# Performance work log

Hardware: AMD Instinct MI355X
Metric: run time of the kernel (lower is better)

## Reference

```python
import jax, jax.numpy as jnp
import numpy as np

D_MODEL = 1024
NUM_HEAD = 16
D_K = D_MODEL // NUM_HEAD
FFN_D = 4096
EPS = 1e-5


def _layernorm(x, gamma, beta):
    mu = jnp.mean(x, axis=-1, keepdims=True)
    var = jnp.mean(jnp.square(x - mu), axis=-1, keepdims=True)
    return (x - mu) * jax.lax.rsqrt(var + EPS) * gamma + beta


def setup_inputs() -> dict:
    key = jax.random.key(0)
    ks = jax.random.split(key, 16)
    s = 1.0 / np.sqrt(D_MODEL)
    sf = 1.0 / np.sqrt(FFN_D)
    # weights stored as [in, out] (transpose of torch nn.Linear.weight)
    return {
        "x": jax.random.normal(ks[0], (4, 2048, D_MODEL), dtype=jnp.float32),
        "wq": jax.random.uniform(ks[1], (D_MODEL, D_MODEL), jnp.float32, -s, s),
        "bq": jax.random.uniform(ks[2], (D_MODEL,), jnp.float32, -s, s),
        "wk": jax.random.uniform(ks[3], (D_MODEL, D_MODEL), jnp.float32, -s, s),
        "bk": jax.random.uniform(ks[4], (D_MODEL,), jnp.float32, -s, s),
        "wv": jax.random.uniform(ks[5], (D_MODEL, D_MODEL), jnp.float32, -s, s),
        "bv": jax.random.uniform(ks[6], (D_MODEL,), jnp.float32, -s, s),
        "wo": jax.random.uniform(ks[7], (D_MODEL, D_MODEL), jnp.float32, -s, s),
        "bo": jax.random.uniform(ks[8], (D_MODEL,), jnp.float32, -s, s),
        "w1": jax.random.uniform(ks[9], (D_MODEL, FFN_D), jnp.float32, -s, s),
        "b1": jax.random.uniform(ks[10], (FFN_D,), jnp.float32, -s, s),
        "w2": jax.random.uniform(ks[11], (FFN_D, D_MODEL), jnp.float32, -sf, sf),
        "b2": jax.random.uniform(ks[12], (D_MODEL,), jnp.float32, -sf, sf),
        "g1": jnp.ones((D_MODEL,), jnp.float32),
        "be1": jnp.zeros((D_MODEL,), jnp.float32),
        "g2": jnp.ones((D_MODEL,), jnp.float32),
        "be2": jnp.zeros((D_MODEL,), jnp.float32),
    }


def reference(x, wq, bq, wk, bk, wv, bv, wo, bo, w1, b1, w2, b2, g1, be1, g2, be2):
    B, S, _ = x.shape
    resid1 = x
    # project and split heads: [B, H, S, d_k]
    def heads(w, b):
        return (x @ w + b).reshape(B, S, NUM_HEAD, D_K).transpose(0, 2, 1, 3)
    q = heads(wq, bq)
    k = heads(wk, bk)
    v = heads(wv, bv)
    scores = jnp.einsum("bhsd,bhtd->bhst", q, k) / jnp.sqrt(jnp.float32(D_K))
    attn = jax.nn.softmax(scores, axis=-1)
    ctx = jnp.einsum("bhst,bhtd->bhsd", attn, v)
    ctx = ctx.transpose(0, 2, 1, 3).reshape(B, S, D_MODEL)
    attn_out = ctx @ wo + bo
    x1 = _layernorm(resid1 + attn_out, g1, be1)
    ffn = jax.nn.relu(x1 @ w1 + b1) @ w2 + b2
    return _layernorm(x1 + ffn, g2, be2)
```

## Files before the change

kernel.cpp:

```cpp
#include <hip/hip_runtime.h>

typedef unsigned short u16;
typedef __attribute__((ext_vector_type(8))) u16 u16x8;
typedef __attribute__((ext_vector_type(8))) __bf16 bf16x8;
typedef __attribute__((ext_vector_type(4))) float floatx4;

#define MFMA16(a, b, c) __builtin_amdgcn_mfma_f32_16x16x32_bf16( \
    __builtin_bit_cast(bf16x8, a), __builtin_bit_cast(bf16x8, b), c, 0, 0, 0)

__device__ __forceinline__ float bf2f(u16 h) {
  unsigned u = ((unsigned)h) << 16;
  float f;
  __builtin_memcpy(&f, &u, 4);
  return f;
}
__device__ __forceinline__ u16 f2bf(float f) {
  unsigned u;
  __builtin_memcpy(&u, &f, 4);
  u += 0x7fff + ((u >> 16) & 1);
  return (u16)(u >> 16);
}
__device__ __forceinline__ u16 f2bf_rtz(float f) {
  unsigned u;
  __builtin_memcpy(&u, &f, 4);
  return (u16)(u >> 16);
}

typedef __attribute__((address_space(1))) const unsigned int gas_u32;
typedef __attribute__((address_space(3))) unsigned int las_u32;

__device__ __forceinline__ void gld_lds16(const u16* g, u16* l) {
  __builtin_amdgcn_global_load_lds((gas_u32*)g, (las_u32*)l, 16, 0, 0);
}

__global__ __launch_bounds__(256) void transpose_k(const float* __restrict__ in,
                                                   u16* __restrict__ out, int R, int C) {
  __shared__ u16 tile[64][65];
  int c0 = blockIdx.x * 64, r0 = blockIdx.y * 64;
  int tc = threadIdx.x & 63, tr = threadIdx.x >> 6;
#pragma unroll
  for (int i = 0; i < 16; ++i)
    tile[tr + i * 4][tc] = f2bf(in[(size_t)(r0 + tr + i * 4) * C + c0 + tc]);
  __syncthreads();
#pragma unroll
  for (int i = 0; i < 16; ++i)
    out[(size_t)(c0 + tr + i * 4) * R + r0 + tc] = tile[tc][tr + i * 4];
}

__global__ __launch_bounds__(256) void vtrans_k(const u16* __restrict__ V,
                                                u16* __restrict__ VtG) {
  __shared__ u16 tile[64][65];
  int t0 = blockIdx.x * 64;
  int bh = blockIdx.y, b = bh >> 4, h = bh & 15;
  int tc = threadIdx.x & 63, tr = threadIdx.x >> 6;
#pragma unroll
  for (int i = 0; i < 16; ++i)
    tile[tr + i * 4][tc] = V[((size_t)(b * 2048 + t0 + tr + i * 4)) * 1024 + h * 64 + tc];
  __syncthreads();
#pragma unroll
  for (int i = 0; i < 16; ++i)
    VtG[((size_t)(bh * 64 + tr + i * 4)) * 2048 + t0 + tc] = tile[tc][tr + i * 4];
}

__global__ __launch_bounds__(256) void convert_k(const float* __restrict__ in,
                                                 u16* __restrict__ out) {
  size_t idx = ((size_t)blockIdx.x * 256 + threadIdx.x) * 8;
  floatx4 f0 = *(const floatx4*)(in + idx);
  floatx4 f1 = *(const floatx4*)(in + idx + 4);
  u16x8 o;
#pragma unroll
  for (int e = 0; e < 4; ++e) o[e] = f2bf(f0[e]);
#pragma unroll
  for (int e = 0; e < 4; ++e) o[4 + e] = f2bf(f1[e]);
  *(u16x8*)(out + idx) = o;
}

template <bool C_F32>
__global__ __launch_bounds__(256, 2) void gemm_bt(const u16* __restrict__ A,
                                                  const u16* __restrict__ BT,
                                                  const float* __restrict__ bias,
                                                  void* __restrict__ Cv, int M, int N, int K,
                                                  int relu) {
  __shared__ __align__(16) u16 As[128 * 32];
  __shared__ __align__(16) u16 Bs[128 * 32];
  const int tid = threadIdx.x, lane = tid & 63, wave = tid >> 6;
  const int quad = lane >> 4, l15 = lane & 15;
  const int wr = wave >> 1, wc = wave & 1;
  const int m0 = blockIdx.x * 128, n0 = blockIdx.y * 128;

  floatx4 acc[4][4] = {};

  for (int k0 = 0; k0 < K; k0 += 32) {
#pragma unroll
    for (int p = 0; p < 2; ++p) {
      int chunk = p * 256 + tid;
      int row = chunk >> 2, cc = chunk & 3;
      int ldsbase = (p * 256 + wave * 64) * 8;
      gld_lds16(A + (size_t)(m0 + row) * K + k0 + cc * 8, As + ldsbase);
      gld_lds16(BT + (size_t)(n0 + row) * K + k0 + cc * 8, Bs + ldsbase);
    }
    __syncthreads();
    u16x8 af[4], bfr[4];
#pragma unroll
    for (int i = 0; i < 4; ++i)
      af[i] = *(const u16x8*)(As + (wr * 64 + i * 16 + l15) * 32 + quad * 8);
#pragma unroll
    for (int j = 0; j < 4; ++j)
      bfr[j] = *(const u16x8*)(Bs + (wc * 64 + j * 16 + l15) * 32 + quad * 8);
#pragma unroll
    for (int i = 0; i < 4; ++i)
#pragma unroll
      for (int j = 0; j < 4; ++j) acc[i][j] = MFMA16(af[i], bfr[j], acc[i][j]);
    __syncthreads();
  }

#pragma unroll
  for (int j = 0; j < 4; ++j) {
    int col = n0 + wc * 64 + j * 16 + l15;
    float bv = bias[col];
#pragma unroll
    for (int i = 0; i < 4; ++i) {
      int row = m0 + wr * 64 + i * 16 + quad * 4;
#pragma unroll
      for (int r = 0; r < 4; ++r) {
        float v = acc[i][j][r] + bv;
        if (relu) v = fmaxf(v, 0.f);
        if (C_F32)
          ((float*)Cv)[(size_t)(row + r) * N + col] = v;
        else
          ((u16*)Cv)[(size_t)(row + r) * N + col] = f2bf(v);
      }
    }
  }
}

__global__ __launch_bounds__(256, 2) void attn_k(const u16* __restrict__ Q,
                                                 const u16* __restrict__ Km,
                                                 const u16* __restrict__ VtG,
                                                 u16* __restrict__ O) {
  __shared__ __align__(16) u16 Qs[128 * 72];
  __shared__ __align__(16) u16 Ks[2][64 * 64];
  __shared__ __align__(16) u16 Vs[2][64 * 64];
  const int tid = threadIdx.x, lane = tid & 63, wave = tid >> 6;
  const int quad = lane >> 4, l15 = lane & 15;
  const int b = blockIdx.z, h = blockIdx.y, q0 = blockIdx.x * 128;
  const int bh = b * 16 + h;
  const size_t tokbase = (size_t)b * 2048;

#pragma unroll
  for (int p = 0; p < 4; ++p) {
    int chunk = p * 256 + tid, row = chunk >> 3, cc = chunk & 7;
    u16x8 qv = *(const u16x8*)(Q + (tokbase + q0 + row) * 1024 + h * 64 + cc * 8);
#pragma unroll
    for (int e = 0; e < 8; ++e) qv[e] = f2bf(bf2f(qv[e]) * 0.125f);
    *(u16x8*)(Qs + row * 72 + cc * 8) = qv;
  }
  __syncthreads();
  u16x8 qa[2][2];
#pragma unroll
  for (int i = 0; i < 2; ++i)
#pragma unroll
    for (int ks = 0; ks < 2; ++ks)
      qa[i][ks] = *(const u16x8*)(Qs + (wave * 32 + i * 16 + l15) * 72 + ks * 32 + quad * 8);
  __syncthreads();
  u16* Ps = Qs;

  floatx4 o[2][4] = {};
  float lsum[2][4] = {};

  auto stage = [&](int it2, int buf) {
    int t0 = it2 * 64;
#pragma unroll
    for (int p = 0; p < 2; ++p) {
      int chunk = p * 256 + tid;
      int row = chunk >> 3, cc = chunk & 7;
      int gc = cc ^ (row & 7);
      int ldsoff = (p * 256 + wave * 64) * 8;
      gld_lds16(Km + (tokbase + t0 + row) * 1024 + h * 64 + gc * 8, &Ks[buf][ldsoff]);
      gld_lds16(VtG + ((size_t)(bh * 64 + row)) * 2048 + t0 + gc * 8, &Vs[buf][ldsoff]);
    }
  };

  stage(0, 0);

  for (int it = 0; it < 32; ++it) {
    const int cur = it & 1;
    __syncthreads();
    if (it + 1 < 32) stage(it + 1, cur ^ 1);

    floatx4 s[2][4] = {};
#pragma unroll
    for (int ks = 0; ks < 2; ++ks) {
      u16x8 kb[4];
#pragma unroll
      for (int j = 0; j < 4; ++j)
        kb[j] = *(const u16x8*)(&Ks[cur][(j * 16 + l15) * 64 + (((ks * 4 + quad) ^ (l15 & 7)) * 8)]);
#pragma unroll
      for (int i = 0; i < 2; ++i)
#pragma unroll
        for (int j = 0; j < 4; ++j) s[i][j] = MFMA16(qa[i][ks], kb[j], s[i][j]);
    }

#pragma unroll
    for (int i = 0; i < 2; ++i)
#pragma unroll
      for (int r = 0; r < 4; ++r) {
        int prow = wave * 32 + i * 16 + quad * 4 + r;
        float ls = 0.f;
#pragma unroll
        for (int j = 0; j < 4; ++j) {
          float p = __expf(s[i][j][r]);
          ls += p;
          Ps[prow * 72 + j * 16 + l15] = f2bf_rtz(p);
        }
        lsum[i][r] += ls;
      }
    asm volatile("s_waitcnt lgkmcnt(0)\n\ts_barrier" ::: "memory");

#pragma unroll
    for (int ks = 0; ks < 2; ++ks) {
      u16x8 pa[2], vbf[4];
#pragma unroll
      for (int i = 0; i < 2; ++i)
        pa[i] = *(const u16x8*)(Ps + (wave * 32 + i * 16 + l15) * 72 + ks * 32 + quad * 8);
#pragma unroll
      for (int jd = 0; jd < 4; ++jd)
        vbf[jd] = *(const u16x8*)(&Vs[cur][(jd * 16 + l15) * 64 + (((ks * 4 + quad) ^ (l15 & 7)) * 8)]);
#pragma unroll
      for (int i = 0; i < 2; ++i)
#pragma unroll
        for (int jd = 0; jd < 4; ++jd) o[i][jd] = MFMA16(pa[i], vbf[jd], o[i][jd]);
    }
  }

#pragma unroll
  for (int i = 0; i < 2; ++i) {
    float inv[4];
#pragma unroll
    for (int r = 0; r < 4; ++r) {
      float v = lsum[i][r];
#pragma unroll
      for (int mk = 1; mk < 16; mk <<= 1) v += __shfl_xor(v, mk);
      inv[r] = 1.0f / fmaxf(v, 1e-30f);
    }
#pragma unroll
    for (int jd = 0; jd < 4; ++jd)
#pragma unroll
      for (int r = 0; r < 4; ++r) {
        float val = o[i][jd][r] * inv[r];
        size_t tok = tokbase + q0 + wave * 32 + i * 16 + quad * 4 + r;
        O[tok * 1024 + h * 64 + jd * 16 + l15] = f2bf(val);
      }
  }
}

template <bool A_F32, bool B_F32, bool OUT_F32>
__global__ __launch_bounds__(256) void ln_k(const void* __restrict__ Av,
                                            const void* __restrict__ Bv,
                                            const float* __restrict__ g,
                                            const float* __restrict__ be,
                                            void* __restrict__ outv) {
  const int lane = threadIdx.x & 63, wave = threadIdx.x >> 6;
  const size_t row = (size_t)blockIdx.x * 4 + wave;
  const size_t base = row * 1024 + lane * 16;
  float v[16];
  if (A_F32) {
    const float* a = (const float*)Av + base;
#pragma unroll
    for (int q = 0; q < 4; ++q) {
      floatx4 t = *(const floatx4*)(a + q * 4);
#pragma unroll
      for (int e = 0; e < 4; ++e) v[q * 4 + e] = t[e];
    }
  } else {
    const u16* a = (const u16*)Av + base;
    u16x8 a0 = *(const u16x8*)a, a1 = *(const u16x8*)(a + 8);
#pragma unroll
    for (int e = 0; e < 8; ++e) {
      v[e] = bf2f(a0[e]);
      v[e + 8] = bf2f(a1[e]);
    }
  }
  if (B_F32) {
    const float* bb = (const float*)Bv + base;
#pragma unroll
    for (int q = 0; q < 4; ++q) {
      floatx4 t = *(const floatx4*)(bb + q * 4);
#pragma unroll
      for (int e = 0; e < 4; ++e) v[q * 4 + e] += t[e];
    }
  } else {
    const u16* bb = (const u16*)Bv + base;
    u16x8 b0 = *(const u16x8*)bb, b1 = *(const u16x8*)(bb + 8);
#pragma unroll
    for (int e = 0; e < 8; ++e) {
      v[e] += bf2f(b0[e]);
      v[e + 8] += bf2f(b1[e]);
    }
  }
  float sum = 0.f, sq = 0.f;
#pragma unroll
  for (int e = 0; e < 16; ++e) {
    sum += v[e];
    sq += v[e] * v[e];
  }
#pragma unroll
  for (int mk = 1; mk < 64; mk <<= 1) {
    sum += __shfl_xor(sum, mk);
    sq += __shfl_xor(sq, mk);
  }
  float mu = sum * (1.f / 1024.f);
  float var = fmaxf(sq * (1.f / 1024.f) - mu * mu, 0.f);
  float rstd = rsqrtf(var + 1e-5f);
  if (OUT_F32) {
    float* o = (float*)outv + base;
#pragma unroll
    for (int q = 0; q < 4; ++q) {
      floatx4 t;
#pragma unroll
      for (int e = 0; e < 4; ++e) {
        int c = lane * 16 + q * 4 + e;
        t[e] = (v[q * 4 + e] - mu) * rstd * g[c] + be[c];
      }
      *(floatx4*)(o + q * 4) = t;
    }
  } else {
    u16x8 o0, o1;
#pragma unroll
    for (int e = 0; e < 8; ++e) {
      int c = lane * 16 + e;
      o0[e] = f2bf((v[e] - mu) * rstd * g[c] + be[c]);
      o1[e] = f2bf((v[e + 8] - mu) * rstd * g[c + 8] + be[c + 8]);
    }
    *(u16x8*)((u16*)outv + base) = o0;
    *(u16x8*)((u16*)outv + base + 8) = o1;
  }
}

extern "C" void kernel_launch(void* const* d_in, const int* in_sizes, int n_in, void* d_out,
                              int out_size, void* d_ws, size_t ws_size, hipStream_t stream) {
  const float* x = (const float*)d_in[0];
  const float* wq = (const float*)d_in[1];
  const float* bq = (const float*)d_in[2];
  const float* wk = (const float*)d_in[3];
  const float* bk = (const float*)d_in[4];
  const float* wv = (const float*)d_in[5];
  const float* bv = (const float*)d_in[6];
  const float* wo = (const float*)d_in[7];
  const float* bo = (const float*)d_in[8];
  const float* w1 = (const float*)d_in[9];
  const float* b1 = (const float*)d_in[10];
  const float* w2 = (const float*)d_in[11];
  const float* b2 = (const float*)d_in[12];
  const float* g1 = (const float*)d_in[13];
  const float* be1 = (const float*)d_in[14];
  const float* g2 = (const float*)d_in[15];
  const float* be2 = (const float*)d_in[16];
  float* out = (float*)d_out;

  u16* W = (u16*)d_ws;
  const size_t M1 = (size_t)1 << 20;
  u16* wqT = W;
  u16* wkT = wqT + M1;
  u16* wvT = wkT + M1;
  u16* woT = wvT + M1;
  u16* w1T = woT + M1;
  u16* w2T = w1T + 4 * M1;
  u16* arena = w2T + 4 * M1;
  const size_t S8M = (size_t)8 << 20;
  u16* xb = arena;
  u16* Qb = arena + S8M;
  u16* Kb = arena + 2 * S8M;
  u16* Vb = arena + 3 * S8M;
  u16* Cb = arena + 4 * S8M;
  u16* VtG = arena + 5 * S8M;
  u16* AO = Qb;
  u16* X1 = xb;
  u16* F1 = Qb;

  dim3 blk(256);
  transpose_k<<<dim3(16, 16), blk, 0, stream>>>(wq, wqT, 1024, 1024);
  transpose_k<<<dim3(16, 16), blk, 0, stream>>>(wk, wkT, 1024, 1024);
  transpose_k<<<dim3(16, 16), blk, 0, stream>>>(wv, wvT, 1024, 1024);
  transpose_k<<<dim3(16, 16), blk, 0, stream>>>(wo, woT, 1024, 1024);
  transpose_k<<<dim3(64, 16), blk, 0, stream>>>(w1, w1T, 1024, 4096);
  transpose_k<<<dim3(16, 64), blk, 0, stream>>>(w2, w2T, 4096, 1024);
  convert_k<<<4096, blk, 0, stream>>>(x, xb);

  gemm_bt<false><<<dim3(64, 8), blk, 0, stream>>>(xb, wqT, bq, Qb, 8192, 1024, 1024, 0);
  gemm_bt<false><<<dim3(64, 8), blk, 0, stream>>>(xb, wkT, bk, Kb, 8192, 1024, 1024, 0);
  gemm_bt<false><<<dim3(64, 8), blk, 0, stream>>>(xb, wvT, bv, Vb, 8192, 1024, 1024, 0);

  vtrans_k<<<dim3(32, 64), blk, 0, stream>>>(Vb, VtG);
  attn_k<<<dim3(16, 16, 4), blk, 0, stream>>>(Qb, Kb, VtG, Cb);

  gemm_bt<false><<<dim3(64, 8), blk, 0, stream>>>(Cb, woT, bo, AO, 8192, 1024, 1024, 0);
  ln_k<true, false, false><<<2048, blk, 0, stream>>>(x, AO, g1, be1, X1);

  gemm_bt<false><<<dim3(64, 32), blk, 0, stream>>>(X1, w1T, b1, F1, 8192, 4096, 1024, 1);
  gemm_bt<true><<<dim3(64, 8), blk, 0, stream>>>(F1, w2T, b2, out, 8192, 1024, 4096, 0);
  ln_k<false, true, true><<<2048, blk, 0, stream>>>(X1, out, g2, be2, out);
}
```

Baseline: 570.9 us.

## Produce transposed V directly from GEMM and enlarge attention query tile

The V projection now computes V^T directly by swapping GEMM operands and adding a row-bias epilogue, so the separate V transpose kernel and its extra buffer go away. The attention kernel processes 256 queries per block instead of 128, which halves K/V reloads per query. It folds log2(e) into the Q scale so softmax can use a raw exp2. It also raises wave priority around the MFMA bursts. The cost is more registers per wave from the larger accumulators, which may hurt occupancy, and fewer attention blocks in the grid.

```diff
diff --git a/kernel.cpp b/kernel.cpp
--- a/kernel.cpp
+++ b/kernel.cpp
@@ -7,6 +7,12 @@
 
 #define MFMA16(a, b, c) __builtin_amdgcn_mfma_f32_16x16x32_bf16( \
     __builtin_bit_cast(bf16x8, a), __builtin_bit_cast(bf16x8, b), c, 0, 0, 0)
+
+#if __has_builtin(__builtin_amdgcn_exp2f)
+#define EXP2(x) __builtin_amdgcn_exp2f(x)
+#else
+#define EXP2(x) exp2f(x)
+#endif
 
 __device__ __forceinline__ float bf2f(u16 h) {
   unsigned u = ((unsigned)h) << 16;
@@ -45,21 +51,6 @@
 #pragma unroll
   for (int i = 0; i < 16; ++i)
     out[(size_t)(c0 + tr + i * 4) * R + r0 + tc] = tile[tc][tr + i * 4];
-}
-
-__global__ __launch_bounds__(256) void vtrans_k(const u16* __restrict__ V,
-                                                u16* __restrict__ VtG) {
-  __shared__ u16 tile[64][65];
-  int t0 = blockIdx.x * 64;
-  int bh = blockIdx.y, b = bh >> 4, h = bh & 15;
-  int tc = threadIdx.x & 63, tr = threadIdx.x >> 6;
-#pragma unroll
-  for (int i = 0; i < 16; ++i)
-    tile[tr + i * 4][tc] = V[((size_t)(b * 2048 + t0 + tr + i * 4)) * 1024 + h * 64 + tc];
-  __syncthreads();
-#pragma unroll
-  for (int i = 0; i < 16; ++i)
-    VtG[((size_t)(bh * 64 + tr + i * 4)) * 2048 + t0 + tc] = tile[tc][tr + i * 4];
 }
 
 __global__ __launch_bounds__(256) void convert_k(const float* __restrict__ in,
@@ -75,7 +66,7 @@
   *(u16x8*)(out + idx) = o;
 }
 
-template <bool C_F32>
+template <bool C_F32, bool BIAS_ROW>
 __global__ __launch_bounds__(256, 2) void gemm_bt(const u16* __restrict__ A,
                                                   const u16* __restrict__ BT,
                                                   const float* __restrict__ bias,
@@ -117,13 +108,13 @@
 #pragma unroll
   for (int j = 0; j < 4; ++j) {
     int col = n0 + wc * 64 + j * 16 + l15;
-    float bv = bias[col];
+    float bv = BIAS_ROW ? 0.f : bias[col];
 #pragma unroll
     for (int i = 0; i < 4; ++i) {
       int row = m0 + wr * 64 + i * 16 + quad * 4;
 #pragma unroll
       for (int r = 0; r < 4; ++r) {
-        float v = acc[i][j][r] + bv;
+        float v = acc[i][j][r] + (BIAS_ROW ? bias[row + r] : bv);
         if (relu) v = fmaxf(v, 0.f);
         if (C_F32)
           ((float*)Cv)[(size_t)(row + r) * N + col] = v;
@@ -136,37 +127,34 @@
 
 __global__ __launch_bounds__(256, 2) void attn_k(const u16* __restrict__ Q,
                                                  const u16* __restrict__ Km,
-                                                 const u16* __restrict__ VtG,
+                                                 const u16* __restrict__ Vt,
                                                  u16* __restrict__ O) {
-  __shared__ __align__(16) u16 Qs[128 * 72];
+  __shared__ __align__(16) u16 Ps[256 * 72];
   __shared__ __align__(16) u16 Ks[2][64 * 64];
   __shared__ __align__(16) u16 Vs[2][64 * 64];
   const int tid = threadIdx.x, lane = tid & 63, wave = tid >> 6;
   const int quad = lane >> 4, l15 = lane & 15;
-  const int b = blockIdx.z, h = blockIdx.y, q0 = blockIdx.x * 128;
-  const int bh = b * 16 + h;
+  const int b = blockIdx.z, h = blockIdx.y, q0 = blockIdx.x * 256;
   const size_t tokbase = (size_t)b * 2048;
 
 #pragma unroll
-  for (int p = 0; p < 4; ++p) {
+  for (int p = 0; p < 8; ++p) {
     int chunk = p * 256 + tid, row = chunk >> 3, cc = chunk & 7;
     u16x8 qv = *(const u16x8*)(Q + (tokbase + q0 + row) * 1024 + h * 64 + cc * 8);
 #pragma unroll
-    for (int e = 0; e < 8; ++e) qv[e] = f2bf(bf2f(qv[e]) * 0.125f);
-    *(u16x8*)(Qs + row * 72 + cc * 8) = qv;
+    for (int e = 0; e < 8; ++e) qv[e] = f2bf(bf2f(qv[e]) * 0.18033688011f);
+    *(u16x8*)(Ps + row * 72 + cc * 8) = qv;
   }
   __syncthreads();
-  u16x8 qa[2][2];
-#pragma unroll
-  for (int i = 0; i < 2; ++i)
+  u16x8 qa[4][2];
+#pragma unroll
+  for (int i = 0; i < 4; ++i)
 #pragma unroll
     for (int ks = 0; ks < 2; ++ks)
-      qa[i][ks] = *(const u16x8*)(Qs + (wave * 32 + i * 16 + l15) * 72 + ks * 32 + quad * 8);
-  __syncthreads();
-  u16* Ps = Qs;
-
-  floatx4 o[2][4] = {};
-  float lsum[2][4] = {};
+      qa[i][ks] = *(const u16x8*)(Ps + (wave * 64 + i * 16 + l15) * 72 + ks * 32 + quad * 8);
+
+  floatx4 o[4][4] = {};
+  float lsum[4][4] = {};
 
   auto stage = [&](int it2, int buf) {
     int t0 = it2 * 64;
@@ -177,7 +165,7 @@
       int gc = cc ^ (row & 7);
       int ldsoff = (p * 256 + wave * 64) * 8;
       gld_lds16(Km + (tokbase + t0 + row) * 1024 + h * 64 + gc * 8, &Ks[buf][ldsoff]);
-      gld_lds16(VtG + ((size_t)(bh * 64 + row)) * 2048 + t0 + gc * 8, &Vs[buf][ldsoff]);
+      gld_lds16(Vt + ((size_t)(h * 64 + row)) * 8192 + tokbase + t0 + gc * 8, &Vs[buf][ldsoff]);
     }
   };
 
@@ -188,28 +176,30 @@
     __syncthreads();
     if (it + 1 < 32) stage(it + 1, cur ^ 1);
 
-    floatx4 s[2][4] = {};
+    floatx4 s[4][4] = {};
 #pragma unroll
     for (int ks = 0; ks < 2; ++ks) {
       u16x8 kb[4];
 #pragma unroll
       for (int j = 0; j < 4; ++j)
         kb[j] = *(const u16x8*)(&Ks[cur][(j * 16 + l15) * 64 + (((ks * 4 + quad) ^ (l15 & 7)) * 8)]);
-#pragma unroll
-      for (int i = 0; i < 2; ++i)
+      __builtin_amdgcn_s_setprio(1);
+#pragma unroll
+      for (int i = 0; i < 4; ++i)
 #pragma unroll
         for (int j = 0; j < 4; ++j) s[i][j] = MFMA16(qa[i][ks], kb[j], s[i][j]);
-    }
-
-#pragma unroll
-    for (int i = 0; i < 2; ++i)
+      __builtin_amdgcn_s_setprio(0);
+    }
+
+#pragma unroll
+    for (int i = 0; i < 4; ++i)
 #pragma unroll
       for (int r = 0; r < 4; ++r) {
-        int prow = wave * 32 + i * 16 + quad * 4 + r;
+        int prow = wave * 64 + i * 16 + quad * 4 + r;
         float ls = 0.f;
 #pragma unroll
         for (int j = 0; j < 4; ++j) {
-          float p = __expf(s[i][j][r]);
+          float p = EXP2(s[i][j][r]);
           ls += p;
           Ps[prow * 72 + j * 16 + l15] = f2bf_rtz(p);
         }
@@ -219,22 +209,24 @@
 
 #pragma unroll
     for (int ks = 0; ks < 2; ++ks) {
-      u16x8 pa[2], vbf[4];
-#pragma unroll
-      for (int i = 0; i < 2; ++i)
-        pa[i] = *(const u16x8*)(Ps + (wave * 32 + i * 16 + l15) * 72 + ks * 32 + quad * 8);
+      u16x8 pa[4], vbf[4];
+#pragma unroll
+      for (int i = 0; i < 4; ++i)
+        pa[i] = *(const u16x8*)(Ps + (wave * 64 + i * 16 + l15) * 72 + ks * 32 + quad * 8);
 #pragma unroll
       for (int jd = 0; jd < 4; ++jd)
         vbf[jd] = *(const u16x8*)(&Vs[cur][(jd * 16 + l15) * 64 + (((ks * 4 + quad) ^ (l15 & 7)) * 8)]);
-#pragma unroll
-      for (int i = 0; i < 2; ++i)
+      __builtin_amdgcn_s_setprio(1);
+#pragma unroll
+      for (int i = 0; i < 4; ++i)
 #pragma unroll
         for (int jd = 0; jd < 4; ++jd) o[i][jd] = MFMA16(pa[i], vbf[jd], o[i][jd]);
-    }
-  }
-
-#pragma unroll
-  for (int i = 0; i < 2; ++i) {
+      __builtin_amdgcn_s_setprio(0);
+    }
+  }
+
+#pragma unroll
+  for (int i = 0; i < 4; ++i) {
     float inv[4];
 #pragma unroll
     for (int r = 0; r < 4; ++r) {
@@ -248,7 +240,7 @@
 #pragma unroll
       for (int r = 0; r < 4; ++r) {
         float val = o[i][jd][r] * inv[r];
-        size_t tok = tokbase + q0 + wave * 32 + i * 16 + quad * 4 + r;
+        size_t tok = tokbase + q0 + wave * 64 + i * 16 + quad * 4 + r;
         O[tok * 1024 + h * 64 + jd * 16 + l15] = f2bf(val);
       }
   }
@@ -371,9 +363,8 @@
   u16* xb = arena;
   u16* Qb = arena + S8M;
   u16* Kb = arena + 2 * S8M;
-  u16* Vb = arena + 3 * S8M;
+  u16* Vtb = arena + 3 * S8M;
   u16* Cb = arena + 4 * S8M;
-  u16* VtG = arena + 5 * S8M;
   u16* AO = Qb;
   u16* X1 = xb;
   u16* F1 = Qb;
@@ -387,17 +378,16 @@
   transpose_k<<<dim3(16, 64), blk, 0, stream>>>(w2, w2T, 4096, 1024);
   convert_k<<<4096, blk, 0, stream>>>(x, xb);
 
-  gemm_bt<false><<<dim3(64, 8), blk, 0, stream>>>(xb, wqT, bq, Qb, 8192, 1024, 1024, 0);
-  gemm_bt<false><<<dim3(64, 8), blk, 0, stream>>>(xb, wkT, bk, Kb, 8192, 1024, 1024, 0);
-  gemm_bt<false><<<dim3(64, 8), blk, 0, stream>>>(xb, wvT, bv, Vb, 8192, 1024, 1024, 0);
-
-  vtrans_k<<<dim3(32, 64), blk, 0, stream>>>(Vb, VtG);
-  attn_k<<<dim3(16, 16, 4), blk, 0, stream>>>(Qb, Kb, VtG, Cb);
-
-  gemm_bt<false><<<dim3(64, 8), blk, 0, stream>>>(Cb, woT, bo, AO, 8192, 1024, 1024, 0);
+  gemm_bt<false, false><<<dim3(64, 8), blk, 0, stream>>>(xb, wqT, bq, Qb, 8192, 1024, 1024, 0);
+  gemm_bt<false, false><<<dim3(64, 8), blk, 0, stream>>>(xb, wkT, bk, Kb, 8192, 1024, 1024, 0);
+  gemm_bt<false, true><<<dim3(8, 64), blk, 0, stream>>>(wvT, xb, bv, Vtb, 1024, 8192, 1024, 0);
+
+  attn_k<<<dim3(8, 16, 4), blk, 0, stream>>>(Qb, Kb, Vtb, Cb);
+
+  gemm_bt<false, false><<<dim3(64, 8), blk, 0, stream>>>(Cb, woT, bo, AO, 8192, 1024, 1024, 0);
   ln_k<true, false, false><<<2048, blk, 0, stream>>>(x, AO, g1, be1, X1);
 
-  gemm_bt<false><<<dim3(64, 32), blk, 0, stream>>>(X1, w1T, b1, F1, 8192, 4096, 1024, 1);
-  gemm_bt<true><<<dim3(64, 8), blk, 0, stream>>>(F1, w2T, b2, out, 8192, 1024, 4096, 0);
+  gemm_bt<false, false><<<dim3(64, 32), blk, 0, stream>>>(X1, w1T, b1, F1, 8192, 4096, 1024, 1);
+  gemm_bt<true, false><<<dim3(64, 8), blk, 0, stream>>>(F1, w2T, b2, out, 8192, 1024, 4096, 0);
   ln_k<false, true, true><<<2048, blk, 0, stream>>>(X1, out, g2, be2, out);
 }
```

Result: no change. 561.5 us (-1.6%).
